# Kernel tuning notes

Hardware: AMD Instinct MI355X
Metric: run time of the kernel (lower is better)

Reference implementation:

```python
import math
import jax, jax.numpy as jnp
import numpy as np

N_ENTITY = 64368
DIM = 128
B = 512
L = 50


def setup_inputs() -> dict:
    key = jax.random.key(0)
    ks = jax.random.split(key, 8)
    entity_emb = jax.random.normal(ks[0], (N_ENTITY, DIM), dtype=jnp.float32) * 0.02
    # SoftAttention params (xavier-like scale)
    W1 = jax.random.normal(ks[1], (DIM, DIM), dtype=jnp.float32) * (1.414 / math.sqrt(DIM))
    W2 = jax.random.normal(ks[2], (DIM, DIM), dtype=jnp.float32) * (1.414 / math.sqrt(DIM))
    q = jax.random.normal(ks[3], (DIM,), dtype=jnp.float32) * (1.414 / math.sqrt(DIM))
    soft_bias = jax.random.normal(ks[4], (), dtype=jnp.float32) * 0.01  # SoftAttention.output.bias (Linear(dim,1))
    out_bias = jax.random.normal(ks[5], (N_ENTITY,), dtype=jnp.float32) * 0.01  # KBRD.output.bias
    seed_sets = jax.random.randint(ks[6], (B, L), 0, N_ENTITY, dtype=jnp.int64)
    labels = jax.random.randint(ks[7], (B,), 0, N_ENTITY, dtype=jnp.int64)
    return {"entity_emb": entity_emb, "W1": W1, "W2": W2, "q": q,
            "soft_bias": soft_bias, "out_bias": out_bias,
            "seed_sets": seed_sets, "labels": labels}


def _positional_encoding(seq_len, dim):
    pos = jnp.arange(seq_len, dtype=jnp.float32)[:, None]            # [L,1]
    div = jnp.exp(jnp.arange(0, dim, 2, dtype=jnp.float32) * (-math.log(10000.0) / dim))  # [D/2]
    pe = jnp.zeros((seq_len, dim), dtype=jnp.float32)
    pe = pe.at[:, 0::2].set(jnp.sin(pos * div) / 1000.0)
    pe = pe.at[:, 1::2].set(jnp.cos(pos * div) / 1000.0)
    return pe  # [L,D]


def reference(entity_emb, W1, W2, q, soft_bias, out_bias, seed_sets, labels):
    dim = entity_emb.shape[1]
    seq_len = seed_sets.shape[1]
    # user_representation: gather seed embeddings + positional encoding (eval: dropout no-op)
    v = entity_emb[seed_sets] + _positional_encoding(seq_len, dim)   # [B,L,D]
    # SoftAttention (note: original applies no softmax over weights)
    vn = v[:, -1, :]                                                 # [B,D]
    inp = jnp.einsum('ed,bld->ble', W1, v) + jnp.einsum('ed,bd->be', W2, vn)[:, None, :] + soft_bias
    att = jnp.einsum('d,bld->bl', q, inp)                            # [B,L]
    u_emb = jnp.einsum('bl,bld->bd', att, v)                         # [B,D]
    # scores = F.linear(u_emb, entity_emb, output.bias)
    scores = u_emb @ entity_emb.T + out_bias                         # [B,N]
    # CrossEntropyLoss (mean)
    logz = jax.nn.logsumexp(scores, axis=1)                          # [B]
    picked = jnp.take_along_axis(scores, labels[:, None], axis=1)[:, 0]
    base_loss = jnp.mean(logz - picked)
    return scores, base_loss
```

## Files before the change

kernel.cpp:

```cpp
#include <hip/hip_runtime.h>
#include <math.h>

#define N_ENT 64368
#define DIM 128
#define BATCH 512
#define SEQ 50

#define WS_QW1 0
#define WS_QW2 128
#define WS_QS  256
#define WS_PE  512
#define WS_PART 7168
#define WS_ABF_BYTES 131072
#define NPART 32

typedef __attribute__((ext_vector_type(8))) short short8;
typedef __attribute__((ext_vector_type(4))) float f32x4;

static __device__ __forceinline__ short f2bf(float f) {
  union { float f; unsigned u; } v;
  v.f = f;
  unsigned r = v.u + 0x7FFF + ((v.u >> 16) & 1);
  return (short)(r >> 16);
}

__global__ __launch_bounds__(512) void prep_kernel(
    const float* __restrict__ W1, const float* __restrict__ W2,
    const float* __restrict__ q, const float* __restrict__ soft_bias,
    float* __restrict__ ws) {
  const int tid = threadIdx.x;
  const int d = tid & 127;
  const int quarter = tid >> 7;

  __shared__ float red1[4][128];
  __shared__ float red2[4][128];
  __shared__ float qsh[128];

  float s1 = 0.f, s2 = 0.f;
  for (int e = quarter * 32; e < quarter * 32 + 32; ++e) {
    float qe = q[e];
    s1 += qe * W1[e * DIM + d];
    s2 += qe * W2[e * DIM + d];
  }
  red1[quarter][d] = s1;
  red2[quarter][d] = s2;
  if (tid < 128) qsh[tid] = q[tid];
  __syncthreads();

  if (tid < 128) {
    ws[WS_QW1 + tid] = red1[0][tid] + red1[1][tid] + red1[2][tid] + red1[3][tid];
    ws[WS_QW2 + tid] = red2[0][tid] + red2[1][tid] + red2[2][tid] + red2[3][tid];
  }
  if (tid == 0) {
    float s = 0.f;
    for (int i = 0; i < 128; ++i) s += qsh[i];
    ws[WS_QS] = soft_bias[0] * s;
  }

  for (int i = tid; i < SEQ * DIM; i += 512) {
    int l = i >> 7, dd = i & 127;
    float div = expf((float)(dd & ~1) * (-logf(10000.0f) / (float)DIM));
    float ang = (float)l * div;
    float v = (dd & 1) ? cosf(ang) : sinf(ang);
    ws[WS_PE + i] = v * 0.001f;
  }
  for (int i = tid; i < NPART * BATCH; i += 512) ws[WS_PART + i] = 0.f;
}

__global__ __launch_bounds__(256) void uemb_kernel(
    const float* __restrict__ emb, const int* __restrict__ seeds,
    const float* __restrict__ ws, short* __restrict__ abf) {
  const int b = blockIdx.x;
  const int tid = threadIdx.x;
  __shared__ float v[SEQ][DIM];
  __shared__ float att[SEQ];
  __shared__ int sidx[SEQ];
  __shared__ float usum[2][DIM];

  if (tid < SEQ) sidx[tid] = seeds[b * SEQ + tid];
  __syncthreads();

  for (int i = tid; i < SEQ * (DIM / 4); i += 256) {
    int l = i >> 5, c4 = i & 31;
    float4 e4 = reinterpret_cast<const float4*>(emb + (size_t)sidx[l] * DIM)[c4];
    float4 p4 = reinterpret_cast<const float4*>(ws + WS_PE + l * DIM)[c4];
    e4.x += p4.x; e4.y += p4.y; e4.z += p4.z; e4.w += p4.w;
    *reinterpret_cast<float4*>(&v[l][c4 * 4]) = e4;
  }
  __syncthreads();

  const int wave = tid >> 6, lane = tid & 63;
  const float qw1a = ws[WS_QW1 + lane], qw1b = ws[WS_QW1 + 64 + lane];
  const float qw2a = ws[WS_QW2 + lane], qw2b = ws[WS_QW2 + 64 + lane];

  float cs = qw2a * v[SEQ - 1][lane] + qw2b * v[SEQ - 1][64 + lane];
#pragma unroll
  for (int m = 32; m; m >>= 1) cs += __shfl_xor(cs, m, 64);
  float c = cs + ws[WS_QS];

  for (int l = wave; l < SEQ; l += 4) {
    float s = qw1a * v[l][lane] + qw1b * v[l][64 + lane];
#pragma unroll
    for (int m = 32; m; m >>= 1) s += __shfl_xor(s, m, 64);
    if (lane == 0) att[l] = s + c;
  }
  __syncthreads();

  const int d = tid & 127, h = tid >> 7;
  float u = 0.f;
  for (int l = h * 25; l < h * 25 + 25; ++l) u += att[l] * v[l][d];
  usum[h][d] = u;
  __syncthreads();
  if (tid < 128) abf[b * DIM + tid] = f2bf(usum[0][tid] + usum[1][tid]);
}

__global__ __launch_bounds__(256) void scores_kernel(
    const float* __restrict__ emb, const float* __restrict__ out_bias,
    const short* __restrict__ abf, float* __restrict__ ws_part,
    float* __restrict__ out) {
  __shared__ float rowpart[BATCH][2];

  const int tid = threadIdx.x;
  const int lane = tid & 63;
  const int wid = tid >> 6;
  const int wr = wid >> 1;
  const int wc = wid & 1;
  const int lrow = lane & 15;
  const int lgrp = lane >> 4;
  const int colBase = blockIdx.x * 64;

  short8 bfrag[2][4];
  float biasv[2];
  bool colok[2];
  int cols[2];
#pragma unroll
  for (int cf = 0; cf < 2; ++cf) {
    int col = colBase + wc * 32 + cf * 16 + lrow;
    cols[cf] = col;
    colok[cf] = (col < N_ENT);
    int e = colok[cf] ? col : (N_ENT - 1);
    biasv[cf] = colok[cf] ? out_bias[col] : 0.f;
#pragma unroll
    for (int ki = 0; ki < 4; ++ki) {
      const float4* p =
          reinterpret_cast<const float4*>(emb + (size_t)e * DIM + ki * 32 + lgrp * 8);
      float4 x0 = p[0];
      float4 x1 = p[1];
      short8 f;
      f[0] = f2bf(x0.x); f[1] = f2bf(x0.y); f[2] = f2bf(x0.z); f[3] = f2bf(x0.w);
      f[4] = f2bf(x1.x); f[5] = f2bf(x1.y); f[6] = f2bf(x1.z); f[7] = f2bf(x1.w);
      bfrag[cf][ki] = f;
    }
  }

  for (int c = 0; c < 8; ++c) {
    const int mBase = c * 64 + wr * 32;

    short8 afrag[2][4];
#pragma unroll
    for (int rf = 0; rf < 2; ++rf)
#pragma unroll
      for (int ki = 0; ki < 4; ++ki) {
        int row = mBase + rf * 16 + lrow;
        afrag[rf][ki] =
            *reinterpret_cast<const short8*>(abf + row * DIM + ki * 32 + lgrp * 8);
      }

    f32x4 acc[2][2];
#pragma unroll
    for (int rf = 0; rf < 2; ++rf)
#pragma unroll
      for (int cf = 0; cf < 2; ++cf)
#pragma unroll
        for (int r = 0; r < 4; ++r) acc[rf][cf][r] = 0.f;

#pragma unroll
    for (int ki = 0; ki < 4; ++ki)
#pragma unroll
      for (int rf = 0; rf < 2; ++rf)
#pragma unroll
        for (int cf = 0; cf < 2; ++cf)
          acc[rf][cf] = __builtin_amdgcn_mfma_f32_16x16x32_bf16(
              afrag[rf][ki], bfrag[cf][ki], acc[rf][cf], 0, 0, 0);

#pragma unroll
    for (int rf = 0; rf < 2; ++rf) {
      float pr[4] = {0.f, 0.f, 0.f, 0.f};
#pragma unroll
      for (int cf = 0; cf < 2; ++cf) {
        if (colok[cf]) {
#pragma unroll
          for (int r = 0; r < 4; ++r) {
            int row = mBase + rf * 16 + lgrp * 4 + r;
            float s = acc[rf][cf][r] + biasv[cf];
            out[(size_t)row * N_ENT + cols[cf]] = s;
            pr[r] += __expf(s);
          }
        }
      }
#pragma unroll
      for (int r = 0; r < 4; ++r) {
#pragma unroll
        for (int m = 1; m < 16; m <<= 1) pr[r] += __shfl_xor(pr[r], m, 64);
      }
      if (lrow == 0) {
#pragma unroll
        for (int r = 0; r < 4; ++r)
          rowpart[mBase + rf * 16 + lgrp * 4 + r][wc] = pr[r];
      }
    }
  }
  __syncthreads();

  const int slot = blockIdx.x & (NPART - 1);
  for (int r = tid; r < BATCH; r += 256) {
    atomicAdd(&ws_part[slot * BATCH + r], rowpart[r][0] + rowpart[r][1]);
  }
}

__global__ __launch_bounds__(512) void loss_kernel(
    const float* __restrict__ scores, const float* __restrict__ ws_part,
    const int* __restrict__ labels, float* __restrict__ out_loss) {
  __shared__ float red[512];
  int t = threadIdx.x;
  float s = 0.f;
#pragma unroll
  for (int p = 0; p < NPART; ++p) s += ws_part[p * BATCH + t];
  float v = logf(s) - scores[(size_t)t * N_ENT + labels[t]];
  red[t] = v;
  __syncthreads();
  for (int off = 256; off > 0; off >>= 1) {
    if (t < off) red[t] += red[t + off];
    __syncthreads();
  }
  if (t == 0) out_loss[0] = red[0] / (float)BATCH;
}

extern "C" void kernel_launch(void* const* d_in, const int* in_sizes, int n_in,
                              void* d_out, int out_size, void* d_ws, size_t ws_size,
                              hipStream_t stream) {
  const float* entity_emb = (const float*)d_in[0];
  const float* W1 = (const float*)d_in[1];
  const float* W2 = (const float*)d_in[2];
  const float* q = (const float*)d_in[3];
  const float* soft_bias = (const float*)d_in[4];
  const float* out_bias = (const float*)d_in[5];
  const int* seeds = (const int*)d_in[6];
  const int* labels = (const int*)d_in[7];
  float* out = (float*)d_out;
  float* ws = (float*)d_ws;
  short* abf = (short*)((char*)d_ws + WS_ABF_BYTES);
  float* ws_part = ws + WS_PART;

  prep_kernel<<<1, 512, 0, stream>>>(W1, W2, q, soft_bias, ws);
  uemb_kernel<<<BATCH, 256, 0, stream>>>(entity_emb, seeds, ws, abf);
  scores_kernel<<<(N_ENT + 63) / 64, 256, 0, stream>>>(entity_emb, out_bias, abf,
                                                       ws_part, out);
  loss_kernel<<<1, 512, 0, stream>>>(out, ws_part, labels,
                                     out + (size_t)BATCH * N_ENT);
}
```

Measured before the change: 204.7 us.

## Fuse prep into uemb kernel and loss into scores via last-block reduction

Removes the single-block prep kernel by having every uemb block recompute q·W1, q·W2 and the positional encoding inline. The loss kernel is folded into the scores kernel: picked logits are accumulated with atomics while scores are written, and the last block to finish (tracked by an atomic counter) does the final logsumexp reduction. Embedding loads and score stores become nontemporal. Two launches and their serial gaps go away, at the cost of redundant per-block matvec work, extra atomics, and a block-completion counter.

```diff
diff --git a/kernel.cpp b/kernel.cpp
--- a/kernel.cpp
+++ b/kernel.cpp
@@ -5,14 +5,12 @@
 #define DIM 128
 #define BATCH 512
 #define SEQ 50
-
-#define WS_QW1 0
-#define WS_QW2 128
-#define WS_QS  256
-#define WS_PE  512
-#define WS_PART 7168
+#define NPART 32
+
+#define WS_PART 0
+#define WS_PICK (NPART * BATCH)
+#define WS_CNT  (NPART * BATCH + 1)
 #define WS_ABF_BYTES 131072
-#define NPART 32
 
 typedef __attribute__((ext_vector_type(8))) short short8;
 typedef __attribute__((ext_vector_type(4))) float f32x4;
@@ -24,82 +22,71 @@
   return (short)(r >> 16);
 }
 
-__global__ __launch_bounds__(512) void prep_kernel(
-    const float* __restrict__ W1, const float* __restrict__ W2,
-    const float* __restrict__ q, const float* __restrict__ soft_bias,
-    float* __restrict__ ws) {
-  const int tid = threadIdx.x;
-  const int d = tid & 127;
-  const int quarter = tid >> 7;
-
-  __shared__ float red1[4][128];
-  __shared__ float red2[4][128];
-  __shared__ float qsh[128];
-
-  float s1 = 0.f, s2 = 0.f;
-  for (int e = quarter * 32; e < quarter * 32 + 32; ++e) {
-    float qe = q[e];
-    s1 += qe * W1[e * DIM + d];
-    s2 += qe * W2[e * DIM + d];
-  }
-  red1[quarter][d] = s1;
-  red2[quarter][d] = s2;
-  if (tid < 128) qsh[tid] = q[tid];
-  __syncthreads();
-
-  if (tid < 128) {
-    ws[WS_QW1 + tid] = red1[0][tid] + red1[1][tid] + red1[2][tid] + red1[3][tid];
-    ws[WS_QW2 + tid] = red2[0][tid] + red2[1][tid] + red2[2][tid] + red2[3][tid];
-  }
-  if (tid == 0) {
-    float s = 0.f;
-    for (int i = 0; i < 128; ++i) s += qsh[i];
-    ws[WS_QS] = soft_bias[0] * s;
-  }
-
-  for (int i = tid; i < SEQ * DIM; i += 512) {
-    int l = i >> 7, dd = i & 127;
-    float div = expf((float)(dd & ~1) * (-logf(10000.0f) / (float)DIM));
-    float ang = (float)l * div;
-    float v = (dd & 1) ? cosf(ang) : sinf(ang);
-    ws[WS_PE + i] = v * 0.001f;
-  }
-  for (int i = tid; i < NPART * BATCH; i += 512) ws[WS_PART + i] = 0.f;
-}
-
-__global__ __launch_bounds__(256) void uemb_kernel(
-    const float* __restrict__ emb, const int* __restrict__ seeds,
-    const float* __restrict__ ws, short* __restrict__ abf) {
+__global__ __launch_bounds__(256) void fused_uemb(
+    const float* __restrict__ emb, const float* __restrict__ W1,
+    const float* __restrict__ W2, const float* __restrict__ q,
+    const float* __restrict__ soft_bias, const int* __restrict__ seeds,
+    float* __restrict__ ws, short* __restrict__ abf) {
   const int b = blockIdx.x;
   const int tid = threadIdx.x;
   __shared__ float v[SEQ][DIM];
+  __shared__ float qw[2][DIM];
   __shared__ float att[SEQ];
   __shared__ int sidx[SEQ];
+  __shared__ float qred[2];
   __shared__ float usum[2][DIM];
-
+  __shared__ float qs_sh;
+
+  if (tid < NPART) ws[WS_PART + b * NPART + tid] = 0.f;
+  if (b == 0 && tid == 0) {
+    ws[WS_PICK] = 0.f;
+    ((int*)ws)[WS_CNT] = 0;
+  }
   if (tid < SEQ) sidx[tid] = seeds[b * SEQ + tid];
-  __syncthreads();
-
+
+  {
+    const int m = tid >> 7, d = tid & 127;
+    const float* __restrict__ W = m ? W2 : W1;
+    float acc = 0.f;
+#pragma unroll 8
+    for (int e = 0; e < DIM; ++e) acc += q[e] * W[e * DIM + d];
+    qw[m][d] = acc;
+    if (m == 0) {
+      float s = q[d];
+#pragma unroll
+      for (int sh = 32; sh; sh >>= 1) s += __shfl_xor(s, sh, 64);
+      if ((tid & 63) == 0) qred[tid >> 6] = s;
+    }
+  }
+  __syncthreads();
+  if (tid == 0) qs_sh = soft_bias[0] * (qred[0] + qred[1]);
+
+  const float kExpScale = -logf(10000.0f) / (float)DIM;
   for (int i = tid; i < SEQ * (DIM / 4); i += 256) {
     int l = i >> 5, c4 = i & 31;
     float4 e4 = reinterpret_cast<const float4*>(emb + (size_t)sidx[l] * DIM)[c4];
-    float4 p4 = reinterpret_cast<const float4*>(ws + WS_PE + l * DIM)[c4];
-    e4.x += p4.x; e4.y += p4.y; e4.z += p4.z; e4.w += p4.w;
-    *reinterpret_cast<float4*>(&v[l][c4 * 4]) = e4;
+    int dd = c4 * 4;
+    float div0 = __expf((float)dd * kExpScale);
+    float div1 = __expf((float)(dd + 2) * kExpScale);
+    float s0, c0, s1, c1;
+    __sincosf((float)l * div0, &s0, &c0);
+    __sincosf((float)l * div1, &s1, &c1);
+    e4.x += s0 * 0.001f;
+    e4.y += c0 * 0.001f;
+    e4.z += s1 * 0.001f;
+    e4.w += c1 * 0.001f;
+    *reinterpret_cast<float4*>(&v[l][dd]) = e4;
   }
   __syncthreads();
 
   const int wave = tid >> 6, lane = tid & 63;
-  const float qw1a = ws[WS_QW1 + lane], qw1b = ws[WS_QW1 + 64 + lane];
-  const float qw2a = ws[WS_QW2 + lane], qw2b = ws[WS_QW2 + 64 + lane];
-
-  float cs = qw2a * v[SEQ - 1][lane] + qw2b * v[SEQ - 1][64 + lane];
+  float cs = qw[1][lane] * v[SEQ - 1][lane] + qw[1][64 + lane] * v[SEQ - 1][64 + lane];
 #pragma unroll
   for (int m = 32; m; m >>= 1) cs += __shfl_xor(cs, m, 64);
-  float c = cs + ws[WS_QS];
+  float c = cs + qs_sh;
 
   for (int l = wave; l < SEQ; l += 4) {
-    float s = qw1a * v[l][lane] + qw1b * v[l][64 + lane];
+    float s = qw[0][lane] * v[l][lane] + qw[0][64 + lane] * v[l][64 + lane];
 #pragma unroll
     for (int m = 32; m; m >>= 1) s += __shfl_xor(s, m, 64);
     if (lane == 0) att[l] = s + c;
@@ -116,9 +103,12 @@
 
 __global__ __launch_bounds__(256) void scores_kernel(
     const float* __restrict__ emb, const float* __restrict__ out_bias,
-    const short* __restrict__ abf, float* __restrict__ ws_part,
-    float* __restrict__ out) {
+    const short* __restrict__ abf, const int* __restrict__ labels,
+    float* __restrict__ ws, float* __restrict__ out) {
   __shared__ float rowpart[BATCH][2];
+  __shared__ int lbl[BATCH];
+  __shared__ int islast_sh;
+  __shared__ float wred[4];
 
   const int tid = threadIdx.x;
   const int lane = tid & 63;
@@ -129,6 +119,8 @@
   const int lgrp = lane >> 4;
   const int colBase = blockIdx.x * 64;
 
+  for (int i = tid; i < BATCH; i += 256) lbl[i] = labels[i];
+
   short8 bfrag[2][4];
   float biasv[2];
   bool colok[2];
@@ -142,16 +134,19 @@
     biasv[cf] = colok[cf] ? out_bias[col] : 0.f;
 #pragma unroll
     for (int ki = 0; ki < 4; ++ki) {
-      const float4* p =
-          reinterpret_cast<const float4*>(emb + (size_t)e * DIM + ki * 32 + lgrp * 8);
-      float4 x0 = p[0];
-      float4 x1 = p[1];
+      const f32x4* p =
+          reinterpret_cast<const f32x4*>(emb + (size_t)e * DIM + ki * 32 + lgrp * 8);
+      f32x4 x0 = __builtin_nontemporal_load(p);
+      f32x4 x1 = __builtin_nontemporal_load(p + 1);
       short8 f;
-      f[0] = f2bf(x0.x); f[1] = f2bf(x0.y); f[2] = f2bf(x0.z); f[3] = f2bf(x0.w);
-      f[4] = f2bf(x1.x); f[5] = f2bf(x1.y); f[6] = f2bf(x1.z); f[7] = f2bf(x1.w);
+      f[0] = f2bf(x0[0]); f[1] = f2bf(x0[1]); f[2] = f2bf(x0[2]); f[3] = f2bf(x0[3]);
+      f[4] = f2bf(x1[0]); f[5] = f2bf(x1[1]); f[6] = f2bf(x1[2]); f[7] = f2bf(x1[3]);
       bfrag[cf][ki] = f;
     }
   }
+  __syncthreads();
+
+  float pickacc = 0.f;
 
   for (int c = 0; c < 8; ++c) {
     const int mBase = c * 64 + wr * 32;
@@ -193,8 +188,9 @@
           for (int r = 0; r < 4; ++r) {
             int row = mBase + rf * 16 + lgrp * 4 + r;
             float s = acc[rf][cf][r] + biasv[cf];
-            out[(size_t)row * N_ENT + cols[cf]] = s;
+            __builtin_nontemporal_store(s, &out[(size_t)row * N_ENT + cols[cf]]);
             pr[r] += __expf(s);
+            if (cols[cf] == lbl[row]) pickacc += s;
           }
         }
       }
@@ -210,30 +206,43 @@
       }
     }
   }
+  if (pickacc != 0.f) atomicAdd(&ws[WS_PICK], pickacc);
   __syncthreads();
 
   const int slot = blockIdx.x & (NPART - 1);
-  for (int r = tid; r < BATCH; r += 256) {
-    atomicAdd(&ws_part[slot * BATCH + r], rowpart[r][0] + rowpart[r][1]);
-  }
-}
-
-__global__ __launch_bounds__(512) void loss_kernel(
-    const float* __restrict__ scores, const float* __restrict__ ws_part,
-    const int* __restrict__ labels, float* __restrict__ out_loss) {
-  __shared__ float red[512];
-  int t = threadIdx.x;
-  float s = 0.f;
-#pragma unroll
-  for (int p = 0; p < NPART; ++p) s += ws_part[p * BATCH + t];
-  float v = logf(s) - scores[(size_t)t * N_ENT + labels[t]];
-  red[t] = v;
-  __syncthreads();
-  for (int off = 256; off > 0; off >>= 1) {
-    if (t < off) red[t] += red[t + off];
+  for (int r = tid; r < BATCH; r += 256)
+    atomicAdd(&ws[WS_PART + slot * BATCH + r], rowpart[r][0] + rowpart[r][1]);
+
+  __threadfence();
+  __syncthreads();
+  if (tid == 0) {
+    int done = atomicAdd((int*)ws + WS_CNT, 1);
+    islast_sh = (done == (int)gridDim.x - 1);
+  }
+  __syncthreads();
+
+  if (islast_sh) {
+    __threadfence();
+    float lsum = 0.f;
+    for (int r = tid; r < BATCH; r += 256) {
+      float rs = 0.f;
+#pragma unroll
+      for (int p = 0; p < NPART; ++p)
+        rs += __hip_atomic_load(&ws[WS_PART + p * BATCH + r], __ATOMIC_RELAXED,
+                                __HIP_MEMORY_SCOPE_AGENT);
+      lsum += __logf(rs);
+    }
+#pragma unroll
+    for (int m = 32; m; m >>= 1) lsum += __shfl_xor(lsum, m, 64);
+    if ((tid & 63) == 0) wred[tid >> 6] = lsum;
     __syncthreads();
-  }
-  if (t == 0) out_loss[0] = red[0] / (float)BATCH;
+    if (tid == 0) {
+      float tot = wred[0] + wred[1] + wred[2] + wred[3];
+      float picked = __hip_atomic_load(&ws[WS_PICK], __ATOMIC_RELAXED,
+                                       __HIP_MEMORY_SCOPE_AGENT);
+      out[(size_t)BATCH * N_ENT] = (tot - picked) / (float)BATCH;
+    }
+  }
 }
 
 extern "C" void kernel_launch(void* const* d_in, const int* in_sizes, int n_in,
@@ -250,12 +259,9 @@
   float* out = (float*)d_out;
   float* ws = (float*)d_ws;
   short* abf = (short*)((char*)d_ws + WS_ABF_BYTES);
-  float* ws_part = ws + WS_PART;
-
-  prep_kernel<<<1, 512, 0, stream>>>(W1, W2, q, soft_bias, ws);
-  uemb_kernel<<<BATCH, 256, 0, stream>>>(entity_emb, seeds, ws, abf);
+
+  fused_uemb<<<BATCH, 256, 0, stream>>>(entity_emb, W1, W2, q, soft_bias, seeds,
+                                        ws, abf);
   scores_kernel<<<(N_ENT + 63) / 64, 256, 0, stream>>>(entity_emb, out_bias, abf,
-                                                       ws_part, out);
-  loss_kernel<<<1, 512, 0, stream>>>(out, ws_part, labels,
-                                     out + (size_t)BATCH * N_ENT);
-}
+                                                       labels, ws, out);
+}
```

New measurement: 323.5 us. 1.58x slower.
